# Performance work log

Measured on AMD Instinct MI355X. Metric: run time of the kernel, lower is better.

Reference implementation:

```python
import jax, jax.numpy as jnp
import numpy as np

STRIDE, PAD, DIL, DG, K = 1, 1, 1, 1, 3  # conv hyperparams from init_kwargs


def setup_inputs() -> dict:
    key = jax.random.key(0)
    k1, k2, k3, k4, k5 = jax.random.split(key, 5)
    N, C, H, W, Co = 8, 128, 96, 96, 128
    K2 = K * K
    x = jax.random.normal(k1, (N, C, H, W), jnp.float32)
    offset = jax.random.normal(k2, (N, 2 * DG * K2, H, W), jnp.float32)
    mask = jax.random.uniform(k3, (N, DG * K2, H, W), jnp.float32)  # post-sigmoid modulation
    weight = jax.random.normal(k4, (Co, C, K, K), jnp.float32) * 0.05
    bias = jax.random.normal(k5, (Co,), jnp.float32) * 0.05
    return {"x": x, "offset": offset, "mask": mask, "weight": weight, "bias": bias}


def modulated_deform_conv2d(x, offset, mask, weight, bias):
    N, C, H, W = x.shape
    Co = weight.shape[0]
    K2 = K * K
    Ho = (H + 2 * PAD - DIL * (K - 1) - 1) // STRIDE + 1
    Wo = (W + 2 * PAD - DIL * (K - 1) - 1) // STRIDE + 1
    Cg = C // DG

    # offsets: [N, dg, K2, 2(y,x), Ho, Wo]; mask: [N, dg, K2, Ho, Wo]
    off = offset.reshape(N, DG, K2, 2, Ho, Wo)
    m = mask.reshape(N, DG, K2, Ho, Wo)

    ky, kx = jnp.meshgrid(jnp.arange(K), jnp.arange(K), indexing="ij")
    ky = ky.reshape(-1).astype(jnp.float32)  # [K2]
    kx = kx.reshape(-1).astype(jnp.float32)
    base_y = (jnp.arange(Ho, dtype=jnp.float32) * STRIDE - PAD)  # [Ho]
    base_x = (jnp.arange(Wo, dtype=jnp.float32) * STRIDE - PAD)  # [Wo]

    # sampling positions: [N, dg, K2, Ho, Wo]
    py = base_y[None, None, None, :, None] + (ky * DIL)[None, None, :, None, None] + off[:, :, :, 0]
    px = base_x[None, None, None, None, :] + (kx * DIL)[None, None, :, None, None] + off[:, :, :, 1]

    y0 = jnp.floor(py)
    x0 = jnp.floor(px)
    wy = (py - y0).reshape(N, DG, 1, -1)  # frac weights, broadcast over Cg
    wx = (px - x0).reshape(N, DG, 1, -1)
    y0i = y0.astype(jnp.int32)
    x0i = x0.astype(jnp.int32)

    xg = x.reshape(N, DG, Cg, H * W)

    def gather(iy, ix):
        valid = ((iy >= 0) & (iy < H) & (ix >= 0) & (ix < W)).reshape(N, DG, 1, -1)
        idx = (jnp.clip(iy, 0, H - 1) * W + jnp.clip(ix, 0, W - 1)).reshape(N, DG, 1, -1)
        v = jnp.take_along_axis(xg, idx, axis=-1)  # [N, dg, Cg, K2*Ho*Wo]
        return v * valid.astype(x.dtype)

    # bilinear with zero padding outside the image
    v = (gather(y0i, x0i) * (1 - wy) * (1 - wx)
         + gather(y0i, x0i + 1) * (1 - wy) * wx
         + gather(y0i + 1, x0i) * wy * (1 - wx)
         + gather(y0i + 1, x0i + 1) * wy * wx)  # [N, dg, Cg, K2*Ho*Wo]

    v = v.reshape(N, DG, Cg, K2, Ho * Wo) * m.reshape(N, DG, 1, K2, Ho * Wo)
    v = v.reshape(N, C, K2, Ho * Wo)

    out = jnp.einsum("nckp,ock->nop", v, weight.reshape(Co, C, K2))
    out = out + bias[None, :, None]
    return out.reshape(N, Co, Ho, Wo)


def reference(x, offset, mask, weight, bias):
    return modulated_deform_conv2d(x, offset, mask, weight, bias)
```

## Files before the change

kernel.cpp:

```cpp
#include <hip/hip_runtime.h>


#define NI 8
#define CI 128
#define HI 96
#define WI 96
#define CO 128
#define K2 9
#define P_TOT 9216
#define TP 64
#define NTILE 144
#define CPAD 40
#define XT_ELEMS ((size_t)NI * P_TOT * CI)
#define WT_ELEMS ((size_t)K2 * CO * CI)
#define WS_NEED ((XT_ELEMS + WT_ELEMS) * 2)
#define PLANE ((size_t)P_TOT * 8)

typedef short short8 __attribute__((ext_vector_type(8)));
typedef float f32x4 __attribute__((ext_vector_type(4)));

static __device__ __forceinline__ ushort bf16_rne(float x) {
    unsigned u = __float_as_uint(x);
    u = (u + 0x7FFF + ((u >> 16) & 1)) >> 16;
    return (ushort)u;
}
static __device__ __forceinline__ unsigned pack_bf2(float a, float b) {
    return (unsigned)bf16_rne(a) | ((unsigned)bf16_rne(b) << 16);
}
static __device__ __forceinline__ unsigned cvt_pk_bf16(float a, float b) {
    unsigned r;
    asm("v_cvt_pk_bf16_f32 %0, %1, %2" : "=v"(r) : "v"(a), "v"(b));
    return r;
}
static __device__ __forceinline__ float bflo(unsigned u) { return __uint_as_float(u << 16); }
static __device__ __forceinline__ float bfhi(unsigned u) { return __uint_as_float(u & 0xFFFF0000u); }

union U4S8 { uint4 u; short8 s; };

static __device__ __forceinline__ void gll16(const ushort* g, ushort* l) {
    __builtin_amdgcn_global_load_lds(
        (const __attribute__((address_space(1))) unsigned int*)g,
        (__attribute__((address_space(3))) unsigned int*)l, 16, 0, 0);
}

__global__ __launch_bounds__(256)
void pre_kernel(const float* __restrict__ x, const float* __restrict__ w,
                ushort* __restrict__ xt, ushort* __restrict__ wt) {
    const int bid = blockIdx.x;
    const int tid = threadIdx.x;
    if (bid < 2304) {
        __shared__ ushort t[64][68];
        const int n = bid / 288, rr = bid % 288;
        const int cblk = rr & 1, hw0 = (rr >> 1) * 64;
        #pragma unroll
        for (int j = 0; j < 4; ++j) {
            int item = j * 256 + tid;
            int c = item >> 4, q = item & 15;
            float4 f = *(const float4*)(x + ((size_t)(n * CI + cblk * 64 + c)) * P_TOT
                                        + hw0 + q * 4);
            t[q * 4 + 0][c] = bf16_rne(f.x);
            t[q * 4 + 1][c] = bf16_rne(f.y);
            t[q * 4 + 2][c] = bf16_rne(f.z);
            t[q * 4 + 3][c] = bf16_rne(f.w);
        }
        __syncthreads();
        #pragma unroll
        for (int j = 0; j < 4; ++j) {
            int item = j * 256 + tid;
            int row = item >> 4, seg = item & 15;
            uint2 v = *(const uint2*)&t[row][seg * 4];
            int chunk = cblk * 8 + (seg >> 1);
            int sub   = (seg & 1) * 4;
            *(uint2*)(xt + ((size_t)n * 16 + chunk) * PLANE
                         + (size_t)(hw0 + row) * 8 + sub) = v;
        }
    } else {
        int s = (bid - 2304) * 256 + tid;
        int k   = s >> 11;
        int r2  = s & 2047;
        int o   = r2 >> 4;
        int csw = r2 & 15;
        int cs  = csw ^ (o & 7);
        const float* src = w + (size_t)o * (CI * K2) + cs * 8 * K2 + k;
        ushort tmp[8];
        #pragma unroll
        for (int j = 0; j < 8; ++j) tmp[j] = bf16_rne(src[j * K2]);
        *(uint4*)&wt[(size_t)s * 8] = *(uint4*)tmp;
    }
}

__global__ __launch_bounds__(256, 3)
void dcn_mfma4_kernel(const ushort* __restrict__ xt,
                      const ushort* __restrict__ wt,
                      const float* __restrict__ offset,
                      const float* __restrict__ mask,
                      const float* __restrict__ bias,
                      float* __restrict__ out)
{
    __shared__ uint2  s_midx[K2 * TP];
    __shared__ float4 s_mw[K2 * TP];
    __shared__ ushort s_w[CO * CI];

    const int tid  = threadIdx.x;
    const int bid  = blockIdx.x;
    const int n    = bid & 7;
    const int tile = bid >> 3;
    const int ty   = tile / 6;
    const int tx   = tile - ty * 6;
    const int wave = tid >> 6;
    const int lane = tid & 63;
    const int l15  = lane & 15;
    const int quad = lane >> 4;

    auto stage = [&](int k) {
        const ushort* g = wt + ((size_t)k * 2048 + wave * 512) * 8;
        ushort* l = &s_w[wave * 512 * 8];
        #pragma unroll
        for (int i = 0; i < 8; ++i)
            gll16(g + (size_t)(i * 64 + lane) * 8, l + i * 64 * 8);
    };

    stage(0);

    for (int itm = 0; itm < 3; ++itm) {
        int item = itm * 256 + tid;
        if (item < K2 * TP) {
            int k = item / TP;
            int i = item % TP;
            int iy = i >> 4, ix = i & 15;
            int ph = ty * 4 + iy;
            int pw = tx * 16 + ix;
            int p  = ph * WI + pw;
            float offy = offset[((size_t)n * (2 * K2) + 2 * k    ) * P_TOT + p];
            float offx = offset[((size_t)n * (2 * K2) + 2 * k + 1) * P_TOT + p];
            float m    = mask  [((size_t)n * K2 + k) * P_TOT + p];
            int ky = k / 3, kx = k % 3;
            float py = (float)(ph - 1 + ky) + offy;
            float px = (float)(pw - 1 + kx) + offx;
            float y0f = floorf(py), x0f = floorf(px);
            float wy = py - y0f, wx = px - x0f;
            int y0 = (int)y0f, x0 = (int)x0f;
            int y1 = y0 + 1,  x1 = x0 + 1;
            bool vy0 = (y0 >= 0) && (y0 < HI);
            bool vy1 = (y1 >= 0) && (y1 < HI);
            bool vx0 = (x0 >= 0) && (x0 < WI);
            bool vx1 = (x1 >= 0) && (x1 < WI);
            unsigned i00 = (vy0 && vx0) ? (unsigned)(y0 * WI + x0) : 0u;
            unsigned i01 = (vy0 && vx1) ? (unsigned)(y0 * WI + x1) : 0u;
            unsigned i10 = (vy1 && vx0) ? (unsigned)(y1 * WI + x0) : 0u;
            unsigned i11 = (vy1 && vx1) ? (unsigned)(y1 * WI + x1) : 0u;
            float w00 = (vy0 && vx0) ? (1.f - wy) * (1.f - wx) * m : 0.f;
            float w01 = (vy0 && vx1) ? (1.f - wy) * wx          * m : 0.f;
            float w10 = (vy1 && vx0) ? wy * (1.f - wx)          * m : 0.f;
            float w11 = (vy1 && vx1) ? wy * wx                  * m : 0.f;
            s_midx[item] = make_uint2(i00 | (i01 << 16), i10 | (i11 << 16));
            s_mw[item]   = make_float4(w00, w01, w10, w11);
        }
    }
    __syncthreads();

    f32x4 acc[8];
    #pragma unroll
    for (int a = 0; a < 8; ++a) acc[a] = (f32x4){0.f, 0.f, 0.f, 0.f};

    const ushort* xp = xt + ((size_t)n * 16 + quad) * PLANE;
    const int mrow = wave * 16 + l15;

    uint4 g0[4], g1[4], g2[4], g3[4];
    float4 mwc;

    auto fetch = [&](int k) {
        uint2 mi = s_midx[k * TP + mrow];
        mwc = s_mw[k * TP + mrow];
        size_t r00 = (size_t)(mi.x & 0xFFFF) * 8;
        size_t r01 = (size_t)(mi.x >> 16)    * 8;
        size_t r10 = (size_t)(mi.y & 0xFFFF) * 8;
        size_t r11 = (size_t)(mi.y >> 16)    * 8;
        #pragma unroll
        for (int cb = 0; cb < 4; ++cb) {
            const ushort* pb = xp + (size_t)cb * 4 * PLANE;
            g0[cb] = *(const uint4*)(pb + r00);
            g1[cb] = *(const uint4*)(pb + r01);
            g2[cb] = *(const uint4*)(pb + r10);
            g3[cb] = *(const uint4*)(pb + r11);
        }
    };

    auto compute = [&]() {
        #pragma unroll
        for (int cb = 0; cb < 4; ++cb) {
            uint4 r0 = g0[cb], r1 = g1[cb], r2 = g2[cb], r3 = g3[cb];
            float v0 = mwc.x * bflo(r0.x) + mwc.y * bflo(r1.x) + mwc.z * bflo(r2.x) + mwc.w * bflo(r3.x);
            float v1 = mwc.x * bfhi(r0.x) + mwc.y * bfhi(r1.x) + mwc.z * bfhi(r2.x) + mwc.w * bfhi(r3.x);
            float v2 = mwc.x * bflo(r0.y) + mwc.y * bflo(r1.y) + mwc.z * bflo(r2.y) + mwc.w * bflo(r3.y);
            float v3 = mwc.x * bfhi(r0.y) + mwc.y * bfhi(r1.y) + mwc.z * bfhi(r2.y) + mwc.w * bfhi(r3.y);
            float v4 = mwc.x * bflo(r0.z) + mwc.y * bflo(r1.z) + mwc.z * bflo(r2.z) + mwc.w * bflo(r3.z);
            float v5 = mwc.x * bfhi(r0.z) + mwc.y * bfhi(r1.z) + mwc.z * bfhi(r2.z) + mwc.w * bfhi(r3.z);
            float v6 = mwc.x * bflo(r0.w) + mwc.y * bflo(r1.w) + mwc.z * bflo(r2.w) + mwc.w * bflo(r3.w);
            float v7 = mwc.x * bfhi(r0.w) + mwc.y * bfhi(r1.w) + mwc.z * bfhi(r2.w) + mwc.w * bfhi(r3.w);
            U4S8 cvt;
            cvt.u.x = cvt_pk_bf16(v0, v1);
            cvt.u.y = cvt_pk_bf16(v2, v3);
            cvt.u.z = cvt_pk_bf16(v4, v5);
            cvt.u.w = cvt_pk_bf16(v6, v7);
            short8 bfr = cvt.s;
            __builtin_amdgcn_s_setprio(1);
            #pragma unroll
            for (int ot = 0; ot < 8; ++ot) {
                int o = ot * 16 + l15;
                short8 afr = *(const short8*)&s_w[o * CI + (((cb * 4 + quad) ^ (o & 7)) * 8)];
                acc[ot] = __builtin_amdgcn_mfma_f32_16x16x32_bf16(afr, bfr, acc[ot], 0, 0, 0);
            }
            __builtin_amdgcn_s_setprio(0);
        }
    };

    fetch(0);

    for (int k = 0; k < K2; ++k) {
        compute();
        if (k < 8) {
            __builtin_amdgcn_s_barrier();
            stage(k + 1);
            __builtin_amdgcn_sched_barrier(0);
            fetch(k + 1);
            __builtin_amdgcn_sched_barrier(0);
            asm volatile("s_waitcnt vmcnt(16)" ::: "memory");
            __builtin_amdgcn_sched_barrier(0);
            __builtin_amdgcn_s_barrier();
        }
    }

    const int pbase = (ty * 4 + wave) * WI + tx * 16 + l15;
    #pragma unroll
    for (int ot = 0; ot < 8; ++ot) {
        #pragma unroll
        for (int r = 0; r < 4; ++r) {
            int o = ot * 16 + quad * 4 + r;
            out[((size_t)n * CO + o) * P_TOT + pbase] = acc[ot][r] + bias[o];
        }
    }
}

__global__ __launch_bounds__(256, 3)
void dcn_fallback_kernel(const float* __restrict__ x,
                         const float* __restrict__ offset,
                         const float* __restrict__ mask,
                         const float* __restrict__ weight,
                         const float* __restrict__ bias,
                         float* __restrict__ out)
{
    __shared__ uint2  s_midx[K2 * TP];
    __shared__ float4 s_mw[K2 * TP];
    __shared__ ushort s_v[TP * CPAD];
    __shared__ ushort s_w[CO * CPAD];

    const int tid  = threadIdx.x;
    const int bid  = blockIdx.x;
    const int n    = bid & 7;
    const int p0   = (bid >> 3) * TP;

    for (int it = 0; it < 3; ++it) {
        int item = it * 256 + tid;
        if (item < K2 * TP) {
            int k = item / TP;
            int i = item % TP;
            int p  = p0 + i;
            int ph = p / WI;
            int pw = p % WI;
            float offy = offset[((size_t)n * (2 * K2) + 2 * k    ) * P_TOT + p];
            float offx = offset[((size_t)n * (2 * K2) + 2 * k + 1) * P_TOT + p];
            float m    = mask  [((size_t)n * K2 + k) * P_TOT + p];
            int ky = k / 3, kx = k % 3;
            float py = (float)(ph - 1 + ky) + offy;
            float px = (float)(pw - 1 + kx) + offx;
            float y0f = floorf(py), x0f = floorf(px);
            float wy = py - y0f, wx = px - x0f;
            int y0 = (int)y0f, x0 = (int)x0f;
            int y1 = y0 + 1,  x1 = x0 + 1;
            bool vy0 = (y0 >= 0) && (y0 < HI);
            bool vy1 = (y1 >= 0) && (y1 < HI);
            bool vx0 = (x0 >= 0) && (x0 < WI);
            bool vx1 = (x1 >= 0) && (x1 < WI);
            unsigned i00 = (vy0 && vx0) ? (unsigned)(y0 * WI + x0) : 0u;
            unsigned i01 = (vy0 && vx1) ? (unsigned)(y0 * WI + x1) : 0u;
            unsigned i10 = (vy1 && vx0) ? (unsigned)(y1 * WI + x0) : 0u;
            unsigned i11 = (vy1 && vx1) ? (unsigned)(y1 * WI + x1) : 0u;
            float w00 = (vy0 && vx0) ? (1.f - wy) * (1.f - wx) * m : 0.f;
            float w01 = (vy0 && vx1) ? (1.f - wy) * wx          * m : 0.f;
            float w10 = (vy1 && vx0) ? wy * (1.f - wx)          * m : 0.f;
            float w11 = (vy1 && vx1) ? wy * wx                  * m : 0.f;
            s_midx[item] = make_uint2(i00 | (i01 << 16), i10 | (i11 << 16));
            s_mw[item]   = make_float4(w00, w01, w10, w11);
        }
    }
    __syncthreads();

    const int wave = tid >> 6;
    const int lane = tid & 63;
    const int l15  = lane & 15;
    const int quad = lane >> 4;
    const int o_base = (wave >> 1) * 64;
    const int p_base = (wave & 1) * 32;
    const int gp = tid & 63;
    const int cg = wave;

    f32x4 acc[4][2];
    #pragma unroll
    for (int a = 0; a < 4; ++a)
        #pragma unroll
        for (int b = 0; b < 2; ++b) acc[a][b] = (f32x4){0.f, 0.f, 0.f, 0.f};

    for (int cb = 0; cb < 4; ++cb) {
        for (int k = 0; k < K2; ++k) {
            {
                uint2  mi = s_midx[k * TP + gp];
                float4 mw = s_mw[k * TP + gp];
                int i00 = mi.x & 0xFFFF, i01 = mi.x >> 16;
                int i10 = mi.y & 0xFFFF, i11 = mi.y >> 16;
                const float* xb = x + ((size_t)(n * CI + cb * 32 + cg * 8)) * (HI * WI);
                float v[8];
                #pragma unroll
                for (int j = 0; j < 8; ++j) {
                    const float* xp = xb + (size_t)j * (HI * WI);
                    v[j] = mw.x * xp[i00] + mw.y * xp[i01]
                         + mw.z * xp[i10] + mw.w * xp[i11];
                }
                uint4 pk;
                pk.x = pack_bf2(v[0], v[1]);
                pk.y = pack_bf2(v[2], v[3]);
                pk.z = pack_bf2(v[4], v[5]);
                pk.w = pack_bf2(v[6], v[7]);
                *(uint4*)&s_v[gp * CPAD + cg * 8] = pk;
            }
            {
                int o = tid >> 1, half = tid & 1;
                const float* wsrc = weight + (size_t)o * (CI * K2)
                                  + (cb * 32 + half * 16) * K2 + k;
                ushort tmp[16];
                #pragma unroll
                for (int i = 0; i < 16; ++i) tmp[i] = bf16_rne(wsrc[i * K2]);
                *(uint4*)&s_w[o * CPAD + half * 16]     = *(uint4*)&tmp[0];
                *(uint4*)&s_w[o * CPAD + half * 16 + 8] = *(uint4*)&tmp[8];
            }
            __syncthreads();
            short8 afr[4], bfr[2];
            #pragma unroll
            for (int ot = 0; ot < 4; ++ot)
                afr[ot] = *(const short8*)&s_w[(o_base + ot * 16 + l15) * CPAD + quad * 8];
            #pragma unroll
            for (int pt = 0; pt < 2; ++pt)
                bfr[pt] = *(const short8*)&s_v[(p_base + pt * 16 + l15) * CPAD + quad * 8];
            #pragma unroll
            for (int ot = 0; ot < 4; ++ot)
                #pragma unroll
                for (int pt = 0; pt < 2; ++pt)
                    acc[ot][pt] = __builtin_amdgcn_mfma_f32_16x16x32_bf16(
                        afr[ot], bfr[pt], acc[ot][pt], 0, 0, 0);
            __syncthreads();
        }
    }

    #pragma unroll
    for (int ot = 0; ot < 4; ++ot)
        #pragma unroll
        for (int r = 0; r < 4; ++r) {
            int o = o_base + ot * 16 + quad * 4 + r;
            float b = bias[o];
            #pragma unroll
            for (int pt = 0; pt < 2; ++pt) {
                int p = p0 + p_base + pt * 16 + l15;
                out[((size_t)n * CO + o) * P_TOT + p] = acc[ot][pt][r] + b;
            }
        }
}

extern "C" void kernel_launch(void* const* d_in, const int* in_sizes, int n_in,
                              void* d_out, int out_size, void* d_ws, size_t ws_size,
                              hipStream_t stream) {
    const float* x      = (const float*)d_in[0];
    const float* offset = (const float*)d_in[1];
    const float* mask   = (const float*)d_in[2];
    const float* weight = (const float*)d_in[3];
    const float* bias   = (const float*)d_in[4];
    float* out = (float*)d_out;

    dim3 block(256);
    if (ws_size >= WS_NEED) {
        ushort* xt = (ushort*)d_ws;
        ushort* wt = xt + XT_ELEMS;
        pre_kernel<<<dim3(2304 + 72), block, 0, stream>>>(x, weight, xt, wt);
        dcn_mfma4_kernel<<<dim3(NI * NTILE), block, 0, stream>>>(
            xt, wt, offset, mask, bias, out);
    } else {
        dcn_fallback_kernel<<<dim3(NI * NTILE), block, 0, stream>>>(
            x, offset, mask, weight, bias, out);
    }
}
```

Measured before the change: 161.7 us.

## Compute bilinear metadata per lane in registers, pipelined one tap ahead

Drops the shared-memory tables of sampling indices and weights that were built in a prologue behind a block-wide sync. Each lane now computes its own indices and weights per kernel tap in registers, with the offset and mask loads prefetched one tap ahead inside the existing pipelined loop. The vmcnt wait is adjusted for the three extra in-flight loads. Freeing the LDS also allows launch bounds to target 4 blocks per CU, which adds register pressure from the extra live values.

```diff
diff --git a/kernel.cpp b/kernel.cpp
--- a/kernel.cpp
+++ b/kernel.cpp
@@ -89,7 +89,7 @@
     }
 }
 
-__global__ __launch_bounds__(256, 3)
+__global__ __launch_bounds__(256, 4)
 void dcn_mfma4_kernel(const ushort* __restrict__ xt,
                       const ushort* __restrict__ wt,
                       const float* __restrict__ offset,
@@ -97,8 +97,6 @@
                       const float* __restrict__ bias,
                       float* __restrict__ out)
 {
-    __shared__ uint2  s_midx[K2 * TP];
-    __shared__ float4 s_mw[K2 * TP];
     __shared__ ushort s_w[CO * CI];
 
     const int tid  = threadIdx.x;
@@ -112,6 +110,10 @@
     const int l15  = lane & 15;
     const int quad = lane >> 4;
 
+    const int ph = ty * 4 + wave;
+    const int pw = tx * 16 + l15;
+    const int p  = ph * WI + pw;
+
     auto stage = [&](int k) {
         const ushort* g = wt + ((size_t)k * 2048 + wave * 512) * 8;
         ushort* l = &s_w[wave * 512 * 8];
@@ -120,62 +122,47 @@
             gll16(g + (size_t)(i * 64 + lane) * 8, l + i * 64 * 8);
     };
 
-    stage(0);
-
-    for (int itm = 0; itm < 3; ++itm) {
-        int item = itm * 256 + tid;
-        if (item < K2 * TP) {
-            int k = item / TP;
-            int i = item % TP;
-            int iy = i >> 4, ix = i & 15;
-            int ph = ty * 4 + iy;
-            int pw = tx * 16 + ix;
-            int p  = ph * WI + pw;
-            float offy = offset[((size_t)n * (2 * K2) + 2 * k    ) * P_TOT + p];
-            float offx = offset[((size_t)n * (2 * K2) + 2 * k + 1) * P_TOT + p];
-            float m    = mask  [((size_t)n * K2 + k) * P_TOT + p];
-            int ky = k / 3, kx = k % 3;
-            float py = (float)(ph - 1 + ky) + offy;
-            float px = (float)(pw - 1 + kx) + offx;
-            float y0f = floorf(py), x0f = floorf(px);
-            float wy = py - y0f, wx = px - x0f;
-            int y0 = (int)y0f, x0 = (int)x0f;
-            int y1 = y0 + 1,  x1 = x0 + 1;
-            bool vy0 = (y0 >= 0) && (y0 < HI);
-            bool vy1 = (y1 >= 0) && (y1 < HI);
-            bool vx0 = (x0 >= 0) && (x0 < WI);
-            bool vx1 = (x1 >= 0) && (x1 < WI);
-            unsigned i00 = (vy0 && vx0) ? (unsigned)(y0 * WI + x0) : 0u;
-            unsigned i01 = (vy0 && vx1) ? (unsigned)(y0 * WI + x1) : 0u;
-            unsigned i10 = (vy1 && vx0) ? (unsigned)(y1 * WI + x0) : 0u;
-            unsigned i11 = (vy1 && vx1) ? (unsigned)(y1 * WI + x1) : 0u;
-            float w00 = (vy0 && vx0) ? (1.f - wy) * (1.f - wx) * m : 0.f;
-            float w01 = (vy0 && vx1) ? (1.f - wy) * wx          * m : 0.f;
-            float w10 = (vy1 && vx0) ? wy * (1.f - wx)          * m : 0.f;
-            float w11 = (vy1 && vx1) ? wy * wx                  * m : 0.f;
-            s_midx[item] = make_uint2(i00 | (i01 << 16), i10 | (i11 << 16));
-            s_mw[item]   = make_float4(w00, w01, w10, w11);
-        }
-    }
-    __syncthreads();
+    auto metaload = [&](int k, float& oy, float& ox, float& mm) {
+        oy = offset[((size_t)n * (2 * K2) + 2 * k    ) * P_TOT + p];
+        ox = offset[((size_t)n * (2 * K2) + 2 * k + 1) * P_TOT + p];
+        mm = mask  [((size_t)n * K2 + k) * P_TOT + p];
+    };
+
+    auto metacalc = [&](int k, float oy, float ox, float mm,
+                        int& i00, int& i01, int& i10, int& i11, float4& mw) {
+        int ky = k / 3, kx = k - ky * 3;
+        float py = (float)(ph - 1 + ky) + oy;
+        float px = (float)(pw - 1 + kx) + ox;
+        float y0f = floorf(py), x0f = floorf(px);
+        float wy = py - y0f, wx = px - x0f;
+        int y0 = (int)y0f, x0 = (int)x0f;
+        int y1 = y0 + 1,  x1 = x0 + 1;
+        bool vy0 = (y0 >= 0) && (y0 < HI);
+        bool vy1 = (y1 >= 0) && (y1 < HI);
+        bool vx0 = (x0 >= 0) && (x0 < WI);
+        bool vx1 = (x1 >= 0) && (x1 < WI);
+        i00 = (vy0 && vx0) ? (y0 * WI + x0) : 0;
+        i01 = (vy0 && vx1) ? (y0 * WI + x1) : 0;
+        i10 = (vy1 && vx0) ? (y1 * WI + x0) : 0;
+        i11 = (vy1 && vx1) ? (y1 * WI + x1) : 0;
+        mw.x = (vy0 && vx0) ? (1.f - wy) * (1.f - wx) * mm : 0.f;
+        mw.y = (vy0 && vx1) ? (1.f - wy) * wx          * mm : 0.f;
+        mw.z = (vy1 && vx0) ? wy * (1.f - wx)          * mm : 0.f;
+        mw.w = (vy1 && vx1) ? wy * wx                  * mm : 0.f;
+    };
 
     f32x4 acc[8];
     #pragma unroll
     for (int a = 0; a < 8; ++a) acc[a] = (f32x4){0.f, 0.f, 0.f, 0.f};
 
     const ushort* xp = xt + ((size_t)n * 16 + quad) * PLANE;
-    const int mrow = wave * 16 + l15;
 
     uint4 g0[4], g1[4], g2[4], g3[4];
     float4 mwc;
 
-    auto fetch = [&](int k) {
-        uint2 mi = s_midx[k * TP + mrow];
-        mwc = s_mw[k * TP + mrow];
-        size_t r00 = (size_t)(mi.x & 0xFFFF) * 8;
-        size_t r01 = (size_t)(mi.x >> 16)    * 8;
-        size_t r10 = (size_t)(mi.y & 0xFFFF) * 8;
-        size_t r11 = (size_t)(mi.y >> 16)    * 8;
+    auto fetch = [&](int i00, int i01, int i10, int i11) {
+        size_t r00 = (size_t)i00 * 8, r01 = (size_t)i01 * 8;
+        size_t r10 = (size_t)i10 * 8, r11 = (size_t)i11 * 8;
         #pragma unroll
         for (int cb = 0; cb < 4; ++cb) {
             const ushort* pb = xp + (size_t)cb * 4 * PLANE;
@@ -215,23 +202,37 @@
         }
     };
 
-    fetch(0);
-
-    for (int k = 0; k < K2; ++k) {
+    stage(0);
+    __builtin_amdgcn_sched_barrier(0);
+    float oyc, oxc, mmc;
+    metaload(0, oyc, oxc, mmc);
+    int i00, i01, i10, i11;
+    metacalc(0, oyc, oxc, mmc, i00, i01, i10, i11, mwc);
+    fetch(i00, i01, i10, i11);
+    float oy1, ox1, mm1;
+    metaload(1, oy1, ox1, mm1);
+    __builtin_amdgcn_s_barrier();
+
+    for (int k = 0; k < 8; ++k) {
         compute();
-        if (k < 8) {
-            __builtin_amdgcn_s_barrier();
-            stage(k + 1);
-            __builtin_amdgcn_sched_barrier(0);
-            fetch(k + 1);
-            __builtin_amdgcn_sched_barrier(0);
-            asm volatile("s_waitcnt vmcnt(16)" ::: "memory");
-            __builtin_amdgcn_sched_barrier(0);
-            __builtin_amdgcn_s_barrier();
-        }
-    }
-
-    const int pbase = (ty * 4 + wave) * WI + tx * 16 + l15;
+        float4 nmw;
+        metacalc(k + 1, oy1, ox1, mm1, i00, i01, i10, i11, nmw);
+        __builtin_amdgcn_s_barrier();
+        stage(k + 1);
+        __builtin_amdgcn_sched_barrier(0);
+        fetch(i00, i01, i10, i11);
+        mwc = nmw;
+        __builtin_amdgcn_sched_barrier(0);
+        int k2 = (k + 2 > 8) ? 8 : k + 2;
+        metaload(k2, oy1, ox1, mm1);
+        __builtin_amdgcn_sched_barrier(0);
+        asm volatile("s_waitcnt vmcnt(19)" ::: "memory");
+        __builtin_amdgcn_sched_barrier(0);
+        __builtin_amdgcn_s_barrier();
+    }
+    compute();
+
+    const int pbase = p;
     #pragma unroll
     for (int ot = 0; ot < 8; ++ot) {
         #pragma unroll
```

Result: no change. 163.1 us (+0.9%).
